# Kernel optimization log

Hardware: AMD Instinct MI355X
Metric: run time of the kernel (lower is better)

The kernel has to match this reference:

```python
import jax, jax.numpy as jnp
import numpy as np

SWIGLU_ALPHA = 1.702
SWIGLU_LIMIT = 7.0
B, S, H, E, K, I = 2, 2048, 2048, 32, 4, 1024


def setup_inputs() -> dict:
    key = jax.random.key(0)
    ks = jax.random.split(key, 8)
    return {
        "hidden_states": jax.random.normal(ks[0], (B, S, H), jnp.float32),
        "gate_w": jax.random.normal(ks[1], (E, H), jnp.float32) * 0.02,
        "gate_b": jnp.zeros((E,), jnp.float32),
        "w_gate": jax.random.normal(ks[2], (E, H, I), jnp.float32) * 0.02,
        "b_gate": jnp.zeros((E, I), jnp.float32),
        "w_up": jax.random.normal(ks[3], (E, H, I), jnp.float32) * 0.02,
        "b_up": jnp.zeros((E, I), jnp.float32),
        "w_down": jax.random.normal(ks[4], (E, I, H), jnp.float32) * 0.02,
        "b_down": jnp.zeros((E, H), jnp.float32),
    }


def reference(hidden_states, gate_w, gate_b, w_gate, b_gate, w_up, b_up, w_down, b_down):
    Bb, Ss, Hh = hidden_states.shape
    x = hidden_states.reshape(-1, Hh)                      # [T, H]
    # --- gate: top-k logits first, then softmax over the selected subset ---
    logits = x @ gate_w.T + gate_b                         # [T, E]
    topk_logits, topk_idx = jax.lax.top_k(logits, K)       # sorted descending
    topk_weight = jax.nn.softmax(topk_logits.astype(jnp.float32), axis=-1)  # [T, K]
    # --- dispatch: replicate each token K times, sort by expert id ---
    flat_idx = topk_idx.reshape(-1)                        # [T*K]
    xs = jnp.repeat(x, K, axis=0)                          # [T*K, H]
    order = jnp.argsort(flat_idx)                          # stable sort by expert
    xt = xs[order]
    gid = flat_idx[order]                                  # expert id per sorted row
    group_sizes = jnp.bincount(flat_idx, length=E).astype(jnp.int32)
    # --- grouped GEMM experts with GPT-OSS SwiGLU ---
    gate = jax.lax.ragged_dot(xt, w_gate, group_sizes) + b_gate[gid]
    up = jax.lax.ragged_dot(xt, w_up, group_sizes) + b_up[gid]
    gate = jnp.minimum(gate, SWIGLU_LIMIT)
    up = jnp.clip(up, -SWIGLU_LIMIT, SWIGLU_LIMIT)
    glu = gate * jax.nn.sigmoid(SWIGLU_ALPHA * gate)
    activated = (up + 1.0) * glu
    outs = jax.lax.ragged_dot(activated, w_down, group_sizes) + b_down[gid]
    # --- unsort and combine with routing weights ---
    inv = jnp.argsort(order)
    outs = outs[inv].reshape(-1, K, Hh)                    # [T, K, H]
    y = jnp.sum(outs * topk_weight[..., None], axis=1).astype(x.dtype)
    return y.reshape(Bb, Ss, Hh)
```

## Files before the change

### kernel.cpp

```cpp
#include <hip/hip_runtime.h>

#define T_TOK 4096
#define E_EXP 32
#define KSEL  4
#define HDIM  2048
#define IDIM  1024
#define TKROW 16384
#define BM    128

typedef __attribute__((ext_vector_type(8))) short   short8;
typedef __attribute__((ext_vector_type(8))) __bf16  bf16x8;
typedef __attribute__((ext_vector_type(4))) float   f32x4;

static __device__ __forceinline__ f32x4 mfma16(short8 a, short8 b, f32x4 c) {
    return __builtin_amdgcn_mfma_f32_16x16x32_bf16(
        __builtin_bit_cast(bf16x8, a), __builtin_bit_cast(bf16x8, b), c, 0, 0, 0);
}

static __device__ __forceinline__ unsigned short f2bf(float f) {
    unsigned u = __builtin_bit_cast(unsigned, f);
    unsigned r = (u + 0x7FFFu + ((u >> 16) & 1u)) >> 16;
    return (unsigned short)r;
}
static __device__ __forceinline__ float bf2f(unsigned short u) {
    return __builtin_bit_cast(float, ((unsigned)u) << 16);
}

__global__ __launch_bounds__(256) void gating_kernel(
    const float* __restrict__ x, const float* __restrict__ gw,
    const float* __restrict__ gb, int* __restrict__ topk_idx,
    float* __restrict__ topk_w)
{
    int wave = threadIdx.x >> 6, lane = threadIdx.x & 63;
    int t = blockIdx.x * 4 + wave;
    const float* xr = x + (size_t)t * HDIM;
    float xv[32];
#pragma unroll
    for (int j = 0; j < 32; j++) xv[j] = xr[lane + 64 * j];
    float logits[E_EXP];
#pragma unroll
    for (int e = 0; e < E_EXP; e++) {
        const float* wr = gw + (size_t)e * HDIM;
        float s = 0.f;
#pragma unroll
        for (int j = 0; j < 32; j++) s = fmaf(xv[j], wr[lane + 64 * j], s);
#pragma unroll
        for (int off = 32; off; off >>= 1) s += __shfl_xor(s, off);
        logits[e] = s + gb[e];
    }
    unsigned sel = 0;
    float v[4]; int id[4];
#pragma unroll
    for (int kk = 0; kk < 4; kk++) {
        float best = -3.4e38f; int bi = 0;
#pragma unroll
        for (int e = 0; e < E_EXP; e++) {
            bool ok = ((sel >> e) & 1u) == 0u;
            bool gt = ok && (logits[e] > best);
            best = gt ? logits[e] : best;
            bi   = gt ? e : bi;
        }
        sel |= 1u << bi; v[kk] = best; id[kk] = bi;
    }
    float m0 = v[0];
    float e0 = __expf(v[0] - m0), e1 = __expf(v[1] - m0);
    float e2 = __expf(v[2] - m0), e3 = __expf(v[3] - m0);
    float inv = 1.f / (e0 + e1 + e2 + e3);
    if (lane == 0) {
        int b4 = t * 4;
        topk_idx[b4 + 0] = id[0]; topk_w[b4 + 0] = e0 * inv;
        topk_idx[b4 + 1] = id[1]; topk_w[b4 + 1] = e1 * inv;
        topk_idx[b4 + 2] = id[2]; topk_w[b4 + 2] = e2 * inv;
        topk_idx[b4 + 3] = id[3]; topk_w[b4 + 3] = e3 * inv;
    }
}

__global__ void init_kernel(int* counts, int* fill) {
    if (threadIdx.x < E_EXP) { counts[threadIdx.x] = 0; fill[threadIdx.x] = 0; }
}

__global__ void histo_kernel(const int* __restrict__ idx, int* counts) {
    int i = blockIdx.x * 256 + threadIdx.x;
    atomicAdd(&counts[idx[i]], 1);
}

__global__ void scan_tiles_kernel(const int* counts, int* offsets,
                                  int* tile_e, int* tile_r, int* ntiles) {
    if (threadIdx.x == 0) {
        int acc = 0;
        for (int e = 0; e < E_EXP; e++) { offsets[e] = acc; acc += counts[e]; }
        offsets[E_EXP] = acc;
        int nt = 0;
        for (int e = 0; e < E_EXP; e++) {
            int c = counts[e];
            for (int r = 0; r < c; r += BM) {
                tile_e[nt] = e; tile_r[nt] = offsets[e] + r; nt++;
            }
        }
        ntiles[0] = nt;
    }
}

__global__ void scatter_kernel(const int* __restrict__ idx, const int* __restrict__ offsets,
                               int* fill, int* __restrict__ pos_of, int* __restrict__ row_tok) {
    int i = blockIdx.x * 256 + threadIdx.x;
    int e = idx[i];
    int pos = offsets[e] + atomicAdd(&fill[e], 1);
    pos_of[i] = pos;
    row_tok[pos] = i >> 2;
}

__global__ __launch_bounds__(64) void gather_kernel(
    const float* __restrict__ x, const int* __restrict__ row_tok,
    unsigned short* __restrict__ xt)
{
    int r = blockIdx.x, lane = threadIdx.x;
    const float4* src = (const float4*)(x + (size_t)row_tok[r] * HDIM);
    unsigned short* dst = xt + (size_t)r * HDIM;
#pragma unroll
    for (int j = 0; j < 8; j++) {
        float4 f = src[lane + 64 * j];
        ushort4 o = make_ushort4(f2bf(f.x), f2bf(f.y), f2bf(f.z), f2bf(f.w));
        *(ushort4*)(dst + 4 * (lane + 64 * j)) = o;
    }
}

__global__ __launch_bounds__(256, 2) void gemm1_kernel(
    const unsigned short* __restrict__ xt, const float* __restrict__ w_gate,
    const float* __restrict__ b_gate, const float* __restrict__ w_up,
    const float* __restrict__ b_up, const int* __restrict__ tile_e,
    const int* __restrict__ tile_r, const int* __restrict__ ntiles,
    const int* __restrict__ offsets, const int* __restrict__ counts,
    unsigned short* __restrict__ act)
{
    int tid = blockIdx.y;
    if (tid >= ntiles[0]) return;
    int e = tile_e[tid], row0 = tile_r[tid];
    int cnt_end = offsets[e] + counts[e];
    int n0 = blockIdx.x * 64;
    __shared__ unsigned short As[128][72];
    __shared__ unsigned short Bg[64][72];
    __shared__ unsigned short Bu[64][72];
    int t = threadIdx.x, lane = t & 63, wave = t >> 6;
    int wr = wave >> 1, wc = wave & 1;
    f32x4 accg[4][2], accu[4][2];
#pragma unroll
    for (int m = 0; m < 4; m++)
#pragma unroll
        for (int n = 0; n < 2; n++) { accg[m][n] = (f32x4)0.f; accu[m][n] = (f32x4)0.f; }

    int arow = t >> 1, akh = (t & 1) * 32;
    int asrcrow = row0 + arow; if (asrcrow > TKROW - 1) asrcrow = TKROW - 1;
    const unsigned short* asrc = xt + (size_t)asrcrow * HDIM + akh;
    int bn = (t & 15) * 4, bk = (t >> 4) * 4;
    const float* wg = w_gate + (size_t)e * HDIM * IDIM + n0 + bn;
    const float* wu = w_up   + (size_t)e * HDIM * IDIM + n0 + bn;
    int lrow = lane & 15, lkh = (lane >> 4) * 8;

    for (int k0 = 0; k0 < HDIM; k0 += 64) {
        short8 a0 = *(const short8*)(asrc + k0);
        short8 a1 = *(const short8*)(asrc + k0 + 8);
        short8 a2 = *(const short8*)(asrc + k0 + 16);
        short8 a3 = *(const short8*)(asrc + k0 + 24);
        float4 g0 = *(const float4*)(wg + (size_t)(k0 + bk + 0) * IDIM);
        float4 g1 = *(const float4*)(wg + (size_t)(k0 + bk + 1) * IDIM);
        float4 g2 = *(const float4*)(wg + (size_t)(k0 + bk + 2) * IDIM);
        float4 g3 = *(const float4*)(wg + (size_t)(k0 + bk + 3) * IDIM);
        float4 u0 = *(const float4*)(wu + (size_t)(k0 + bk + 0) * IDIM);
        float4 u1 = *(const float4*)(wu + (size_t)(k0 + bk + 1) * IDIM);
        float4 u2 = *(const float4*)(wu + (size_t)(k0 + bk + 2) * IDIM);
        float4 u3 = *(const float4*)(wu + (size_t)(k0 + bk + 3) * IDIM);
        __syncthreads();
        *(short8*)&As[arow][akh]      = a0;
        *(short8*)&As[arow][akh + 8]  = a1;
        *(short8*)&As[arow][akh + 16] = a2;
        *(short8*)&As[arow][akh + 24] = a3;
        *(ushort4*)&Bg[bn + 0][bk] = make_ushort4(f2bf(g0.x), f2bf(g1.x), f2bf(g2.x), f2bf(g3.x));
        *(ushort4*)&Bg[bn + 1][bk] = make_ushort4(f2bf(g0.y), f2bf(g1.y), f2bf(g2.y), f2bf(g3.y));
        *(ushort4*)&Bg[bn + 2][bk] = make_ushort4(f2bf(g0.z), f2bf(g1.z), f2bf(g2.z), f2bf(g3.z));
        *(ushort4*)&Bg[bn + 3][bk] = make_ushort4(f2bf(g0.w), f2bf(g1.w), f2bf(g2.w), f2bf(g3.w));
        *(ushort4*)&Bu[bn + 0][bk] = make_ushort4(f2bf(u0.x), f2bf(u1.x), f2bf(u2.x), f2bf(u3.x));
        *(ushort4*)&Bu[bn + 1][bk] = make_ushort4(f2bf(u0.y), f2bf(u1.y), f2bf(u2.y), f2bf(u3.y));
        *(ushort4*)&Bu[bn + 2][bk] = make_ushort4(f2bf(u0.z), f2bf(u1.z), f2bf(u2.z), f2bf(u3.z));
        *(ushort4*)&Bu[bn + 3][bk] = make_ushort4(f2bf(u0.w), f2bf(u1.w), f2bf(u2.w), f2bf(u3.w));
        __syncthreads();
#pragma unroll
        for (int kk = 0; kk < 2; kk++) {
            short8 af[4], bgf[2], buf_[2];
#pragma unroll
            for (int m = 0; m < 4; m++)
                af[m] = *(const short8*)&As[wr * 64 + m * 16 + lrow][kk * 32 + lkh];
#pragma unroll
            for (int n = 0; n < 2; n++) {
                bgf[n]  = *(const short8*)&Bg[wc * 32 + n * 16 + lrow][kk * 32 + lkh];
                buf_[n] = *(const short8*)&Bu[wc * 32 + n * 16 + lrow][kk * 32 + lkh];
            }
#pragma unroll
            for (int m = 0; m < 4; m++)
#pragma unroll
                for (int n = 0; n < 2; n++) {
                    accg[m][n] = mfma16(af[m], bgf[n], accg[m][n]);
                    accu[m][n] = mfma16(af[m], buf_[n], accu[m][n]);
                }
        }
    }
#pragma unroll
    for (int n = 0; n < 2; n++) {
        int gcol = n0 + wc * 32 + n * 16 + lrow;
        float bgv = b_gate[e * IDIM + gcol];
        float buv = b_up[e * IDIM + gcol];
#pragma unroll
        for (int m = 0; m < 4; m++) {
            int rb = row0 + wr * 64 + m * 16 + (lane >> 4) * 4;
#pragma unroll
            for (int r = 0; r < 4; r++) {
                int grow = rb + r;
                if (grow < cnt_end) {
                    float gv = accg[m][n][r] + bgv;
                    float uv = accu[m][n][r] + buv;
                    gv = fminf(gv, 7.f);
                    uv = fminf(fmaxf(uv, -7.f), 7.f);
                    float glu = gv / (1.f + __expf(-1.702f * gv));
                    float av = (uv + 1.f) * glu;
                    act[(size_t)grow * IDIM + gcol] = f2bf(av);
                }
            }
        }
    }
}

__global__ __launch_bounds__(256, 2) void gemm2_kernel(
    const unsigned short* __restrict__ act, const float* __restrict__ w_down,
    const float* __restrict__ b_down, const int* __restrict__ tile_e,
    const int* __restrict__ tile_r, const int* __restrict__ ntiles,
    const int* __restrict__ offsets, const int* __restrict__ counts,
    unsigned short* __restrict__ outs)
{
    int tid = blockIdx.y;
    if (tid >= ntiles[0]) return;
    int e = tile_e[tid], row0 = tile_r[tid];
    int cnt_end = offsets[e] + counts[e];
    int n0 = blockIdx.x * 64;
    __shared__ unsigned short As[128][72];
    __shared__ unsigned short Bs[64][72];
    int t = threadIdx.x, lane = t & 63, wave = t >> 6;
    int wr = wave >> 1, wc = wave & 1;
    f32x4 acc[4][2];
#pragma unroll
    for (int m = 0; m < 4; m++)
#pragma unroll
        for (int n = 0; n < 2; n++) acc[m][n] = (f32x4)0.f;

    int arow = t >> 1, akh = (t & 1) * 32;
    int asrcrow = row0 + arow; if (asrcrow > TKROW - 1) asrcrow = TKROW - 1;
    const unsigned short* asrc = act + (size_t)asrcrow * IDIM + akh;
    int bn = (t & 15) * 4, bk = (t >> 4) * 4;
    const float* wd = w_down + (size_t)e * IDIM * HDIM + n0 + bn;
    int lrow = lane & 15, lkh = (lane >> 4) * 8;

    for (int k0 = 0; k0 < IDIM; k0 += 64) {
        short8 a0 = *(const short8*)(asrc + k0);
        short8 a1 = *(const short8*)(asrc + k0 + 8);
        short8 a2 = *(const short8*)(asrc + k0 + 16);
        short8 a3 = *(const short8*)(asrc + k0 + 24);
        float4 g0 = *(const float4*)(wd + (size_t)(k0 + bk + 0) * HDIM);
        float4 g1 = *(const float4*)(wd + (size_t)(k0 + bk + 1) * HDIM);
        float4 g2 = *(const float4*)(wd + (size_t)(k0 + bk + 2) * HDIM);
        float4 g3 = *(const float4*)(wd + (size_t)(k0 + bk + 3) * HDIM);
        __syncthreads();
        *(short8*)&As[arow][akh]      = a0;
        *(short8*)&As[arow][akh + 8]  = a1;
        *(short8*)&As[arow][akh + 16] = a2;
        *(short8*)&As[arow][akh + 24] = a3;
        *(ushort4*)&Bs[bn + 0][bk] = make_ushort4(f2bf(g0.x), f2bf(g1.x), f2bf(g2.x), f2bf(g3.x));
        *(ushort4*)&Bs[bn + 1][bk] = make_ushort4(f2bf(g0.y), f2bf(g1.y), f2bf(g2.y), f2bf(g3.y));
        *(ushort4*)&Bs[bn + 2][bk] = make_ushort4(f2bf(g0.z), f2bf(g1.z), f2bf(g2.z), f2bf(g3.z));
        *(ushort4*)&Bs[bn + 3][bk] = make_ushort4(f2bf(g0.w), f2bf(g1.w), f2bf(g2.w), f2bf(g3.w));
        __syncthreads();
#pragma unroll
        for (int kk = 0; kk < 2; kk++) {
            short8 af[4], bf[2];
#pragma unroll
            for (int m = 0; m < 4; m++)
                af[m] = *(const short8*)&As[wr * 64 + m * 16 + lrow][kk * 32 + lkh];
#pragma unroll
            for (int n = 0; n < 2; n++)
                bf[n] = *(const short8*)&Bs[wc * 32 + n * 16 + lrow][kk * 32 + lkh];
#pragma unroll
            for (int m = 0; m < 4; m++)
#pragma unroll
                for (int n = 0; n < 2; n++)
                    acc[m][n] = mfma16(af[m], bf[n], acc[m][n]);
        }
    }
#pragma unroll
    for (int n = 0; n < 2; n++) {
        int gcol = n0 + wc * 32 + n * 16 + lrow;
        float bdv = b_down[e * HDIM + gcol];
#pragma unroll
        for (int m = 0; m < 4; m++) {
            int rb = row0 + wr * 64 + m * 16 + (lane >> 4) * 4;
#pragma unroll
            for (int r = 0; r < 4; r++) {
                int grow = rb + r;
                if (grow < cnt_end)
                    outs[(size_t)grow * HDIM + gcol] = f2bf(acc[m][n][r] + bdv);
            }
        }
    }
}

__global__ __launch_bounds__(256) void combine_kernel(
    const unsigned short* __restrict__ outs, const int* __restrict__ pos_of,
    const float* __restrict__ topk_w, float* __restrict__ y)
{
    int tok = blockIdx.x;
    int c0 = threadIdx.x * 8;
    float acc[8] = {0.f, 0.f, 0.f, 0.f, 0.f, 0.f, 0.f, 0.f};
#pragma unroll
    for (int k = 0; k < 4; k++) {
        int pos = pos_of[tok * 4 + k];
        float w = topk_w[tok * 4 + k];
        short8 vv = *(const short8*)(outs + (size_t)pos * HDIM + c0);
#pragma unroll
        for (int j = 0; j < 8; j++)
            acc[j] = fmaf(w, bf2f((unsigned short)vv[j]), acc[j]);
    }
    float4 o0 = make_float4(acc[0], acc[1], acc[2], acc[3]);
    float4 o1 = make_float4(acc[4], acc[5], acc[6], acc[7]);
    *(float4*)(y + (size_t)tok * HDIM + c0)     = o0;
    *(float4*)(y + (size_t)tok * HDIM + c0 + 4) = o1;
}

extern "C" void kernel_launch(void* const* d_in, const int* in_sizes, int n_in,
                              void* d_out, int out_size, void* d_ws, size_t ws_size,
                              hipStream_t stream) {
    const float* x      = (const float*)d_in[0];
    const float* gw     = (const float*)d_in[1];
    const float* gb     = (const float*)d_in[2];
    const float* w_gate = (const float*)d_in[3];
    const float* b_gate = (const float*)d_in[4];
    const float* w_up   = (const float*)d_in[5];
    const float* b_up   = (const float*)d_in[6];
    const float* w_down = (const float*)d_in[7];
    const float* b_down = (const float*)d_in[8];
    float* y = (float*)d_out;

    char* base = (char*)d_ws;
    size_t off = 0;
    int*   topk_idx = (int*)(base + off);   off += (size_t)TKROW * 4;
    float* topk_w   = (float*)(base + off); off += (size_t)TKROW * 4;
    int*   counts   = (int*)(base + off);   off += 256;
    int*   offsets  = (int*)(base + off);   off += 256;
    int*   fill     = (int*)(base + off);   off += 256;
    int*   ntiles   = (int*)(base + off);   off += 256;
    int*   tile_e   = (int*)(base + off);   off += 1024;
    int*   tile_r   = (int*)(base + off);   off += 1024;
    int*   pos_of   = (int*)(base + off);   off += (size_t)TKROW * 4;
    int*   row_tok  = (int*)(base + off);   off += (size_t)TKROW * 4;
    unsigned short* xt   = (unsigned short*)(base + off); off += (size_t)TKROW * HDIM * 2;
    unsigned short* act  = (unsigned short*)(base + off); off += (size_t)TKROW * IDIM * 2;
    unsigned short* outs = (unsigned short*)(base + off); off += (size_t)TKROW * HDIM * 2;

    init_kernel<<<1, 64, 0, stream>>>(counts, fill);
    gating_kernel<<<T_TOK / 4, 256, 0, stream>>>(x, gw, gb, topk_idx, topk_w);
    histo_kernel<<<TKROW / 256, 256, 0, stream>>>(topk_idx, counts);
    scan_tiles_kernel<<<1, 64, 0, stream>>>(counts, offsets, tile_e, tile_r, ntiles);
    scatter_kernel<<<TKROW / 256, 256, 0, stream>>>(topk_idx, offsets, fill, pos_of, row_tok);
    gather_kernel<<<TKROW, 64, 0, stream>>>(x, row_tok, xt);
    gemm1_kernel<<<dim3(IDIM / 64, 160), 256, 0, stream>>>(
        xt, w_gate, b_gate, w_up, b_up, tile_e, tile_r, ntiles, offsets, counts, act);
    gemm2_kernel<<<dim3(HDIM / 64, 160), 256, 0, stream>>>(
        act, w_down, b_down, tile_e, tile_r, ntiles, offsets, counts, outs);
    combine_kernel<<<T_TOK, 256, 0, stream>>>(outs, pos_of, topk_w, y);
}
```

Before: 686.7 us.

## Prefetch next K-tile into registers, XOR-swizzle LDS, use packed bf16 convert

Both expert GEMM kernels now issue the global loads for the next K-tile into registers after storing the current tile to LDS. This lets memory latency overlap with the MFMA loop instead of stalling at the top of each iteration. The padded LDS arrays are replaced by unpadded ones with an XOR swizzle to avoid bank conflicts, which also cuts LDS footprint. The manual fp32→bf16 rounding is replaced by the hardware v_cvt_pk_bf16_f32 instruction in the GEMMs and the gather. The register prefetch raises register pressure, which could hurt occupancy under the 2-block launch bound.

```diff
diff --git a/kernel.cpp b/kernel.cpp
--- a/kernel.cpp
+++ b/kernel.cpp
@@ -24,6 +24,11 @@
 }
 static __device__ __forceinline__ float bf2f(unsigned short u) {
     return __builtin_bit_cast(float, ((unsigned)u) << 16);
+}
+static __device__ __forceinline__ unsigned cvtpk(float lo, float hi) {
+    unsigned r;
+    asm("v_cvt_pk_bf16_f32 %0, %1, %2" : "=v"(r) : "v"(lo), "v"(hi));
+    return r;
 }
 
 __global__ __launch_bounds__(256) void gating_kernel(
@@ -115,13 +120,15 @@
     unsigned short* __restrict__ xt)
 {
     int r = blockIdx.x, lane = threadIdx.x;
-    const float4* src = (const float4*)(x + (size_t)row_tok[r] * HDIM);
+    const f32x4* src = (const f32x4*)(x + (size_t)row_tok[r] * HDIM);
     unsigned short* dst = xt + (size_t)r * HDIM;
 #pragma unroll
     for (int j = 0; j < 8; j++) {
-        float4 f = src[lane + 64 * j];
-        ushort4 o = make_ushort4(f2bf(f.x), f2bf(f.y), f2bf(f.z), f2bf(f.w));
-        *(ushort4*)(dst + 4 * (lane + 64 * j)) = o;
+        f32x4 f = src[lane + 64 * j];
+        uint2 o;
+        o.x = cvtpk(f[0], f[1]);
+        o.y = cvtpk(f[2], f[3]);
+        *(uint2*)(dst + 4 * (lane + 64 * j)) = o;
     }
 }
 
@@ -138,9 +145,9 @@
     int e = tile_e[tid], row0 = tile_r[tid];
     int cnt_end = offsets[e] + counts[e];
     int n0 = blockIdx.x * 64;
-    __shared__ unsigned short As[128][72];
-    __shared__ unsigned short Bg[64][72];
-    __shared__ unsigned short Bu[64][72];
+    __shared__ unsigned short As[128 * 64];
+    __shared__ unsigned short Bg[64 * 64];
+    __shared__ unsigned short Bu[64 * 64];
     int t = threadIdx.x, lane = t & 63, wave = t >> 6;
     int wr = wave >> 1, wc = wave & 1;
     f32x4 accg[4][2], accu[4][2];
@@ -150,60 +157,67 @@
         for (int n = 0; n < 2; n++) { accg[m][n] = (f32x4)0.f; accu[m][n] = (f32x4)0.f; }
 
     int arow = t >> 1, akh = (t & 1) * 32;
-    int asrcrow = row0 + arow; if (asrcrow > TKROW - 1) asrcrow = TKROW - 1;
-    const unsigned short* asrc = xt + (size_t)asrcrow * HDIM + akh;
+    int asr = row0 + arow; if (asr > TKROW - 1) asr = TKROW - 1;
+    const unsigned short* ap = xt + (size_t)asr * HDIM + akh;
+    int aw  = arow * 64 + akh;
+    int axk = ((arow >> 2) & 3) << 4;
     int bn = (t & 15) * 4, bk = (t >> 4) * 4;
-    const float* wg = w_gate + (size_t)e * HDIM * IDIM + n0 + bn;
-    const float* wu = w_up   + (size_t)e * HDIM * IDIM + n0 + bn;
-    int lrow = lane & 15, lkh = (lane >> 4) * 8;
-
+    size_t wbase = (size_t)e * ((size_t)HDIM * IDIM) + (size_t)bk * IDIM + n0 + bn;
+    const float* gp = w_gate + wbase;
+    const float* upp = w_up + wbase;
+    int bxk = (t & 3) << 4;
+    int lrow = lane & 15, lg8 = (lane >> 4) * 8;
+    int rxk = ((lrow >> 2) & 3) << 4;
+
+    short8 aR[4]; f32x4 gR[4], uR[4];
+#define LOAD_T1() do { \
+    aR[0] = *(const short8*)(ap);      aR[1] = *(const short8*)(ap + 8);  \
+    aR[2] = *(const short8*)(ap + 16); aR[3] = *(const short8*)(ap + 24); \
+    gR[0] = *(const f32x4*)(gp);                 gR[1] = *(const f32x4*)(gp + IDIM);      \
+    gR[2] = *(const f32x4*)(gp + 2 * IDIM);      gR[3] = *(const f32x4*)(gp + 3 * IDIM);  \
+    uR[0] = *(const f32x4*)(upp);                uR[1] = *(const f32x4*)(upp + IDIM);     \
+    uR[2] = *(const f32x4*)(upp + 2 * IDIM);     uR[3] = *(const f32x4*)(upp + 3 * IDIM); \
+    ap += 64; gp += (size_t)64 * IDIM; upp += (size_t)64 * IDIM; } while (0)
+
+    LOAD_T1();
     for (int k0 = 0; k0 < HDIM; k0 += 64) {
-        short8 a0 = *(const short8*)(asrc + k0);
-        short8 a1 = *(const short8*)(asrc + k0 + 8);
-        short8 a2 = *(const short8*)(asrc + k0 + 16);
-        short8 a3 = *(const short8*)(asrc + k0 + 24);
-        float4 g0 = *(const float4*)(wg + (size_t)(k0 + bk + 0) * IDIM);
-        float4 g1 = *(const float4*)(wg + (size_t)(k0 + bk + 1) * IDIM);
-        float4 g2 = *(const float4*)(wg + (size_t)(k0 + bk + 2) * IDIM);
-        float4 g3 = *(const float4*)(wg + (size_t)(k0 + bk + 3) * IDIM);
-        float4 u0 = *(const float4*)(wu + (size_t)(k0 + bk + 0) * IDIM);
-        float4 u1 = *(const float4*)(wu + (size_t)(k0 + bk + 1) * IDIM);
-        float4 u2 = *(const float4*)(wu + (size_t)(k0 + bk + 2) * IDIM);
-        float4 u3 = *(const float4*)(wu + (size_t)(k0 + bk + 3) * IDIM);
         __syncthreads();
-        *(short8*)&As[arow][akh]      = a0;
-        *(short8*)&As[arow][akh + 8]  = a1;
-        *(short8*)&As[arow][akh + 16] = a2;
-        *(short8*)&As[arow][akh + 24] = a3;
-        *(ushort4*)&Bg[bn + 0][bk] = make_ushort4(f2bf(g0.x), f2bf(g1.x), f2bf(g2.x), f2bf(g3.x));
-        *(ushort4*)&Bg[bn + 1][bk] = make_ushort4(f2bf(g0.y), f2bf(g1.y), f2bf(g2.y), f2bf(g3.y));
-        *(ushort4*)&Bg[bn + 2][bk] = make_ushort4(f2bf(g0.z), f2bf(g1.z), f2bf(g2.z), f2bf(g3.z));
-        *(ushort4*)&Bg[bn + 3][bk] = make_ushort4(f2bf(g0.w), f2bf(g1.w), f2bf(g2.w), f2bf(g3.w));
-        *(ushort4*)&Bu[bn + 0][bk] = make_ushort4(f2bf(u0.x), f2bf(u1.x), f2bf(u2.x), f2bf(u3.x));
-        *(ushort4*)&Bu[bn + 1][bk] = make_ushort4(f2bf(u0.y), f2bf(u1.y), f2bf(u2.y), f2bf(u3.y));
-        *(ushort4*)&Bu[bn + 2][bk] = make_ushort4(f2bf(u0.z), f2bf(u1.z), f2bf(u2.z), f2bf(u3.z));
-        *(ushort4*)&Bu[bn + 3][bk] = make_ushort4(f2bf(u0.w), f2bf(u1.w), f2bf(u2.w), f2bf(u3.w));
+#pragma unroll
+        for (int j = 0; j < 4; j++)
+            *(short8*)&As[(aw + 8 * j) ^ axk] = aR[j];
+#pragma unroll
+        for (int j = 0; j < 4; j++) {
+            uint2 vg, vu;
+            vg.x = cvtpk(gR[0][j], gR[1][j]); vg.y = cvtpk(gR[2][j], gR[3][j]);
+            vu.x = cvtpk(uR[0][j], uR[1][j]); vu.y = cvtpk(uR[2][j], uR[3][j]);
+            int r = bn + j;
+            *(uint2*)&Bg[(r * 64 + bk) ^ bxk] = vg;
+            *(uint2*)&Bu[(r * 64 + bk) ^ bxk] = vu;
+        }
+        if (k0 + 64 < HDIM) LOAD_T1();
         __syncthreads();
 #pragma unroll
         for (int kk = 0; kk < 2; kk++) {
-            short8 af[4], bgf[2], buf_[2];
+            short8 af[4], bgf[2], buf2[2];
 #pragma unroll
             for (int m = 0; m < 4; m++)
-                af[m] = *(const short8*)&As[wr * 64 + m * 16 + lrow][kk * 32 + lkh];
+                af[m] = *(const short8*)&As[((wr * 64 + m * 16 + lrow) * 64 + kk * 32 + lg8) ^ rxk];
 #pragma unroll
             for (int n = 0; n < 2; n++) {
-                bgf[n]  = *(const short8*)&Bg[wc * 32 + n * 16 + lrow][kk * 32 + lkh];
-                buf_[n] = *(const short8*)&Bu[wc * 32 + n * 16 + lrow][kk * 32 + lkh];
+                int rb = (wc * 32 + n * 16 + lrow) * 64 + kk * 32 + lg8;
+                bgf[n]  = *(const short8*)&Bg[rb ^ rxk];
+                buf2[n] = *(const short8*)&Bu[rb ^ rxk];
             }
 #pragma unroll
             for (int m = 0; m < 4; m++)
 #pragma unroll
                 for (int n = 0; n < 2; n++) {
                     accg[m][n] = mfma16(af[m], bgf[n], accg[m][n]);
-                    accu[m][n] = mfma16(af[m], buf_[n], accu[m][n]);
+                    accu[m][n] = mfma16(af[m], buf2[n], accu[m][n]);
                 }
         }
     }
+#undef LOAD_T1
 #pragma unroll
     for (int n = 0; n < 2; n++) {
         int gcol = n0 + wc * 32 + n * 16 + lrow;
@@ -241,8 +255,8 @@
     int e = tile_e[tid], row0 = tile_r[tid];
     int cnt_end = offsets[e] + counts[e];
     int n0 = blockIdx.x * 64;
-    __shared__ unsigned short As[128][72];
-    __shared__ unsigned short Bs[64][72];
+    __shared__ unsigned short As[128 * 64];
+    __shared__ unsigned short Bs[64 * 64];
     int t = threadIdx.x, lane = t & 63, wave = t >> 6;
     int wr = wave >> 1, wc = wave & 1;
     f32x4 acc[4][2];
@@ -252,40 +266,48 @@
         for (int n = 0; n < 2; n++) acc[m][n] = (f32x4)0.f;
 
     int arow = t >> 1, akh = (t & 1) * 32;
-    int asrcrow = row0 + arow; if (asrcrow > TKROW - 1) asrcrow = TKROW - 1;
-    const unsigned short* asrc = act + (size_t)asrcrow * IDIM + akh;
+    int asr = row0 + arow; if (asr > TKROW - 1) asr = TKROW - 1;
+    const unsigned short* ap = act + (size_t)asr * IDIM + akh;
+    int aw  = arow * 64 + akh;
+    int axk = ((arow >> 2) & 3) << 4;
     int bn = (t & 15) * 4, bk = (t >> 4) * 4;
-    const float* wd = w_down + (size_t)e * IDIM * HDIM + n0 + bn;
-    int lrow = lane & 15, lkh = (lane >> 4) * 8;
-
+    const float* gp = w_down + (size_t)e * ((size_t)IDIM * HDIM) + (size_t)bk * HDIM + n0 + bn;
+    int bxk = (t & 3) << 4;
+    int lrow = lane & 15, lg8 = (lane >> 4) * 8;
+    int rxk = ((lrow >> 2) & 3) << 4;
+
+    short8 aR[4]; f32x4 gR[4];
+#define LOAD_T2() do { \
+    aR[0] = *(const short8*)(ap);      aR[1] = *(const short8*)(ap + 8);  \
+    aR[2] = *(const short8*)(ap + 16); aR[3] = *(const short8*)(ap + 24); \
+    gR[0] = *(const f32x4*)(gp);                 gR[1] = *(const f32x4*)(gp + HDIM);      \
+    gR[2] = *(const f32x4*)(gp + 2 * HDIM);      gR[3] = *(const f32x4*)(gp + 3 * HDIM);  \
+    ap += 64; gp += (size_t)64 * HDIM; } while (0)
+
+    LOAD_T2();
     for (int k0 = 0; k0 < IDIM; k0 += 64) {
-        short8 a0 = *(const short8*)(asrc + k0);
-        short8 a1 = *(const short8*)(asrc + k0 + 8);
-        short8 a2 = *(const short8*)(asrc + k0 + 16);
-        short8 a3 = *(const short8*)(asrc + k0 + 24);
-        float4 g0 = *(const float4*)(wd + (size_t)(k0 + bk + 0) * HDIM);
-        float4 g1 = *(const float4*)(wd + (size_t)(k0 + bk + 1) * HDIM);
-        float4 g2 = *(const float4*)(wd + (size_t)(k0 + bk + 2) * HDIM);
-        float4 g3 = *(const float4*)(wd + (size_t)(k0 + bk + 3) * HDIM);
         __syncthreads();
-        *(short8*)&As[arow][akh]      = a0;
-        *(short8*)&As[arow][akh + 8]  = a1;
-        *(short8*)&As[arow][akh + 16] = a2;
-        *(short8*)&As[arow][akh + 24] = a3;
-        *(ushort4*)&Bs[bn + 0][bk] = make_ushort4(f2bf(g0.x), f2bf(g1.x), f2bf(g2.x), f2bf(g3.x));
-        *(ushort4*)&Bs[bn + 1][bk] = make_ushort4(f2bf(g0.y), f2bf(g1.y), f2bf(g2.y), f2bf(g3.y));
-        *(ushort4*)&Bs[bn + 2][bk] = make_ushort4(f2bf(g0.z), f2bf(g1.z), f2bf(g2.z), f2bf(g3.z));
-        *(ushort4*)&Bs[bn + 3][bk] = make_ushort4(f2bf(g0.w), f2bf(g1.w), f2bf(g2.w), f2bf(g3.w));
+#pragma unroll
+        for (int j = 0; j < 4; j++)
+            *(short8*)&As[(aw + 8 * j) ^ axk] = aR[j];
+#pragma unroll
+        for (int j = 0; j < 4; j++) {
+            uint2 vg;
+            vg.x = cvtpk(gR[0][j], gR[1][j]); vg.y = cvtpk(gR[2][j], gR[3][j]);
+            int r = bn + j;
+            *(uint2*)&Bs[(r * 64 + bk) ^ bxk] = vg;
+        }
+        if (k0 + 64 < IDIM) LOAD_T2();
         __syncthreads();
 #pragma unroll
         for (int kk = 0; kk < 2; kk++) {
             short8 af[4], bf[2];
 #pragma unroll
             for (int m = 0; m < 4; m++)
-                af[m] = *(const short8*)&As[wr * 64 + m * 16 + lrow][kk * 32 + lkh];
+                af[m] = *(const short8*)&As[((wr * 64 + m * 16 + lrow) * 64 + kk * 32 + lg8) ^ rxk];
 #pragma unroll
             for (int n = 0; n < 2; n++)
-                bf[n] = *(const short8*)&Bs[wc * 32 + n * 16 + lrow][kk * 32 + lkh];
+                bf[n] = *(const short8*)&Bs[((wc * 32 + n * 16 + lrow) * 64 + kk * 32 + lg8) ^ rxk];
 #pragma unroll
             for (int m = 0; m < 4; m++)
 #pragma unroll
@@ -293,6 +315,7 @@
                     acc[m][n] = mfma16(af[m], bf[n], acc[m][n]);
         }
     }
+#undef LOAD_T2
 #pragma unroll
     for (int n = 0; n < 2; n++) {
         int gcol = n0 + wc * 32 + n * 16 + lrow;
```

Result: no change. 686.0 us (-0.1%).
